# Performance work log

Hardware: AMD Instinct MI355X
Metric: run time of the kernel (lower is better)

The kernel has to match this reference:

```python
import jax, jax.numpy as jnp
import numpy as np

M = 1024      # mol_dim
H = 1024      # ffn_hidden
T = 2048      # sequence length
NS = 5        # n_solvents
DE = 64       # desc_emb_dim
NB = 3        # ffn/residual blocks
HIN = 2 * M + DE + 1  # beta head input dim


def setup_inputs() -> dict:
    key = jax.random.key(0)
    ks = jax.random.split(key, 32)
    w = lambda i, shape: (0.02 * jax.random.normal(ks[i], shape, dtype=jnp.float32))
    inp = {
        "mol_vec": jax.random.normal(ks[0], (M,), dtype=jnp.float32),
        "solvent_seq": jax.random.uniform(ks[1], (T, NS), dtype=jnp.float32),
        "desc_seq": jax.random.normal(ks[2], (T, 6), dtype=jnp.float32),
        "solvent_vecs": jax.random.normal(ks[3], (NS, M), dtype=jnp.float32),
        "boundary_mask": jnp.zeros((T,), dtype=bool),
        # SolventProjection: Linear(5*M -> M) + 3 residual FFN blocks
        "sp_proj_w": w(4, (NS * M, M)), "sp_proj_b": jnp.zeros((M,), jnp.float32),
        "sp_fc1_w": w(5, (NB, M, M)), "sp_fc1_b": jnp.zeros((NB, M), jnp.float32),
        "sp_fc2_w": w(6, (NB, M, M)), "sp_fc2_b": jnp.zeros((NB, M), jnp.float32),
        "sp_ln_g": jnp.ones((NB, M), jnp.float32), "sp_ln_b": jnp.zeros((NB, M), jnp.float32),
        # desc_proj: Linear(6 -> 64)
        "desc_w": w(7, (6, DE)), "desc_b": jnp.zeros((DE,), jnp.float32),
        "bh_proj_w": w(8, (HIN, H)), "bh_proj_b": jnp.zeros((H,), jnp.float32),
        "bh_fc1_w": w(9, (NB, H, H)), "bh_fc1_b": jnp.zeros((NB, H), jnp.float32),
        "bh_fc2_w": w(10, (NB, H, H)), "bh_fc2_b": jnp.zeros((NB, H), jnp.float32),
        "bh_ln_g": jnp.ones((NB, H), jnp.float32), "bh_ln_b": jnp.zeros((NB, H), jnp.float32),
        "mu_w": w(11, (H,)), "mu_b": jnp.zeros((1,), jnp.float32),
        "phi_w": w(12, (H,)), "phi_b": jnp.zeros((1,), jnp.float32),
    }
    return inp


def _gelu(x):
    return jax.nn.gelu(x, approximate=False)  # torch nn.GELU default (erf)


def _ln(x, g, b, eps=1e-5):
    m = jnp.mean(x, axis=-1, keepdims=True)
    v = jnp.mean((x - m) ** 2, axis=-1, keepdims=True)
    return g * (x - m) * jax.lax.rsqrt(v + eps) + b


def _res_blocks(x, w1, b1, w2, b2, g, b):
    # stack of ResidualFFNBlock (dropout=0 / eval mode)
    for i in range(w1.shape[0]):
        x = _ln(_gelu(x @ w1[i] + b1[i]) @ w2[i] + b2[i] + x, g[i], b[i])
    return x


def reference(mol_vec, solvent_seq, desc_seq, solvent_vecs, boundary_mask,
              sp_proj_w, sp_proj_b, sp_fc1_w, sp_fc1_b, sp_fc2_w, sp_fc2_b, sp_ln_g, sp_ln_b,
              desc_w, desc_b,
              bh_proj_w, bh_proj_b, bh_fc1_w, bh_fc1_b, bh_fc2_w, bh_fc2_b, bh_ln_g, bh_ln_b,
              mu_w, mu_b, phi_w, phi_b):
    def step(prev_rf, xs):
        ratios, desc, is_b = xs  # [5], [6], scalar bool
        # SolventProjection: scale each solvent vec by its ratio, concat, project
        sv = (solvent_vecs * ratios[:, None]).reshape(-1)         # [5*M]
        sp = _gelu(sv @ sp_proj_w + sp_proj_b)                     # [M]
        sp = _res_blocks(sp, sp_fc1_w, sp_fc1_b, sp_fc2_w, sp_fc2_b, sp_ln_g, sp_ln_b)
        demb = _gelu(desc @ desc_w + desc_b)                       # [DE]
        x = jnp.concatenate([mol_vec, sp, demb, prev_rf[None]])   # [HIN]
        z = _gelu(x @ bh_proj_w + bh_proj_b)                       # [H]
        z = _res_blocks(z, bh_fc1_w, bh_fc1_b, bh_fc2_w, bh_fc2_b, bh_ln_g, bh_ln_b)
        mu = jax.nn.sigmoid(jnp.dot(z, mu_w) + mu_b[0])
        phi = jax.nn.softplus(jnp.dot(z, phi_w) + phi_b[0]) + 2.0
        # monotonic update: restart at system boundaries or before first prediction
        rf = jnp.where(is_b | (prev_rf < 0), mu, prev_rf + mu * (1.0 - prev_rf))
        return jax.lax.stop_gradient(rf), (rf, mu, phi)  # prev_rf is detached in torch

    prev0 = jnp.float32(-1.0)
    _, (rfs, mus, phis) = jax.lax.scan(step, prev0, (solvent_seq, desc_seq, boundary_mask))
    return jnp.stack([rfs, mus, phis])  # [3, T]
```

## Files before the change

### kernel.cpp

```cpp
#include <hip/hip_runtime.h>
#include <math.h>

#define MDIM 1024
#define TSEQ 2048
#define NSOL 5
#define DED  64
#define NBLK 3
#define KITER 2
#define XLDB 1088
#define NRED 14336
#define RST  64

typedef __bf16 bf16x8 __attribute__((ext_vector_type(8)));
typedef __bf16 bf16x4 __attribute__((ext_vector_type(4)));
typedef float  f32x4  __attribute__((ext_vector_type(4)));

#define GLDS16(gptr, lptr) __builtin_amdgcn_global_load_lds( \
    (const __attribute__((address_space(1))) unsigned int*)(const void*)(gptr), \
    (__attribute__((address_space(3))) unsigned int*)(void*)(lptr), 16, 0, 0)

__device__ __forceinline__ float gelu_f(float x){
  return 0.5f * x * (1.0f + erff(x * 0.70710678118654752440f));
}
__device__ __forceinline__ float sigmoid_f(float x){ return 1.0f/(1.0f+expf(-x)); }
__device__ __forceinline__ float softplus_f(float x){ return fmaxf(x,0.0f) + log1pf(expf(-fabsf(x))); }

__global__ __launch_bounds__(256) void k_cvtT13(const float* __restrict__ s0,
    const float* __restrict__ s1, const float* __restrict__ s2, const float* __restrict__ s3,
    const float* __restrict__ s4, __bf16* __restrict__ dst, __bf16* __restrict__ WpT,
    const float* __restrict__ spg, const float* __restrict__ bhg){
  __shared__ float t[32][33];
  const size_t MM = (size_t)MDIM*MDIM;
  int z = blockIdx.z;
  int tx = threadIdx.x & 31, ty = threadIdx.x >> 5;
  if (z < 12){
    if (blockIdx.y >= 32) return;
    const float* s = (z<3)? s0 + (size_t)z*MM : (z<6)? s1 + (size_t)(z-3)*MM :
                     (z<9)? s2 + (size_t)(z-6)*MM : s3 + (size_t)(z-9)*MM;
    const float* gf = (z==1)? spg : (z==2)? spg+MDIM : (z==7)? bhg : (z==8)? bhg+MDIM : nullptr;
    __bf16* d = dst + (size_t)z*MM;
    int k0 = blockIdx.y*32, n0 = blockIdx.x*32;
    #pragma unroll
    for (int r=0;r<32;r+=8){
      float val = s[(size_t)(k0+ty+r)*MDIM + n0+tx];
      if (gf) val *= gf[k0+ty+r];
      t[ty+r][tx] = val;
    }
    __syncthreads();
    #pragma unroll
    for (int r=0;r<32;r+=8) d[(size_t)(n0+ty+r)*MDIM + k0+tx] = (__bf16)t[tx][ty+r];
  } else {
    int k0 = blockIdx.y*32, n0 = blockIdx.x*32;
    #pragma unroll
    for (int r=0;r<32;r+=8) t[ty+r][tx] = s4[(size_t)(k0+ty+r)*MDIM + n0+tx];
    __syncthreads();
    #pragma unroll
    for (int r=0;r<32;r+=8) WpT[(size_t)(n0+ty+r)*XLDB + k0+tx] = (__bf16)t[tx][ty+r];
  }
}

__global__ __launch_bounds__(256) void k_pm(const float* __restrict__ sv,
    const float* __restrict__ spW, const float* __restrict__ mol,
    const float* __restrict__ bhw, float* __restrict__ PART,
    const float* __restrict__ spfc1w, const float* __restrict__ bhfc1w,
    const float* __restrict__ splg, const float* __restrict__ splb,
    const float* __restrict__ bhlg, const float* __restrict__ bhlb){
  const size_t MM = (size_t)MDIM*MDIM;
  int s = blockIdx.y;
  int j = blockIdx.x*256 + threadIdx.x;
  int z = blockIdx.z, k0 = z*64;
  if (s < NSOL){
    const float* w = spW + (size_t)s*MM + (size_t)k0*MDIM + j;
    const float* v = sv + s*MDIM + k0;
    float acc = 0.f;
    for (int k=0;k<64;k++) acc = fmaf(v[k], w[(size_t)k*MDIM], acc);
    PART[(size_t)z*NRED + s*MDIM + j] = acc;
  } else if (s == NSOL){
    const float* w = bhw + (size_t)k0*MDIM + j;
    float acc = 0.f;
    for (int k=0;k<64;k++) acc = fmaf(mol[k0+k], w[(size_t)k*MDIM], acc);
    PART[(size_t)z*NRED + 5120 + j] = acc;
  } else {
    int m = s - 6;
    const float* W = (m<2)? spfc1w + (size_t)(m+1)*MM : bhfc1w + (size_t)(m-1)*MM;
    const float* g = (m<2)? splg + m*MDIM : bhlg + (m-2)*MDIM;
    const float* b = (m<2)? splb + m*MDIM : bhlb + (m-2)*MDIM;
    float aS=0.f, aB=0.f;
    for (int k=0;k<64;k++){
      float w = W[(size_t)(k0+k)*MDIM + j];
      aS = fmaf(g[k0+k], w, aS);
      aB = fmaf(b[k0+k], w, aB);
    }
    PART[(size_t)z*NRED + 6144 + m*2048 + j] = aS;
    PART[(size_t)z*NRED + 6144 + m*2048 + 1024 + j] = aB;
  }
}

__global__ __launch_bounds__(256) void k_red(const float* __restrict__ PART,
    const float* __restrict__ bhb, float* __restrict__ P, float* __restrict__ mp,
    float* __restrict__ prevg, int* __restrict__ dlist, int* __restrict__ dcnt,
    const float* __restrict__ spfc1b, const float* __restrict__ bhfc1b,
    float* __restrict__ S1buf, float* __restrict__ biasF){
  int i = blockIdx.x*256 + threadIdx.x;
  if (i < TSEQ){ prevg[i] = (i==0)? -1.0f : 1.0f; dlist[i] = i; }
  if (i == 0) *dcnt = TSEQ;
  float a = 0.f;
  #pragma unroll
  for (int z=0;z<16;z++) a += PART[(size_t)z*NRED + i];
  if (i < 5120) P[i] = a;
  else if (i < 6144) mp[i-5120] = a + bhb[i-5120];
  else {
    int off = i - 6144, m = off>>11, r = off&2047;
    if (r < 1024) S1buf[(m<<10)+r] = a;
    else {
      const float* b1 = ((m<2)? spfc1b : bhfc1b) + (((m&1)+1)<<10);
      biasF[(m<<10)+(r-1024)] = a + b1[r-1024];
    }
  }
}

__global__ __launch_bounds__(256) void k_sp0d(const float* __restrict__ ratios,
    const float* __restrict__ P, const float* __restrict__ bias,
    const float* __restrict__ desc, const float* __restrict__ dw,
    const float* __restrict__ db, __bf16* __restrict__ Xb){
  int t = blockIdx.y;
  if (blockIdx.x < 4){
    int j = blockIdx.x*256 + threadIdx.x;
    const float* r = ratios + t*NSOL;
    float acc = bias[j];
    #pragma unroll
    for (int s=0;s<NSOL;s++) acc = fmaf(r[s], P[s*MDIM+j], acc);
    Xb[(size_t)t*XLDB + j] = (__bf16)gelu_f(acc);
  } else if (threadIdx.x < DED){
    int e = threadIdx.x;
    const float* d = desc + t*6;
    float acc = db[e];
    #pragma unroll
    for (int c=0;c<6;c++) acc = fmaf(d[c], dw[c*DED+e], acc);
    Xb[(size_t)t*XLDB + MDIM + e] = (__bf16)gelu_f(acc);
  }
}

template<int BK, bool GELU, bool RES, bool RESLN, bool OUTF, bool OUTB, bool Z0, bool LNFOLD, bool STATS>
__global__ __launch_bounds__(512) void k_mfma_gemm(
    const __bf16* __restrict__ A, int lda, int K,
    const __bf16* __restrict__ Bt,
    const float* __restrict__ bias,
    const __bf16* __restrict__ R, int ldr,
    float* __restrict__ Cf, int ldcf,
    __bf16* __restrict__ Cb, int ldcb,
    const float* __restrict__ wlast, const float* __restrict__ prevg,
    __bf16* __restrict__ Z0b,
    const float* __restrict__ pSin, const float* __restrict__ pQin,
    float* __restrict__ pSout, float* __restrict__ pQout,
    const float* __restrict__ S1, const float* __restrict__ biasF,
    const float* __restrict__ lng, const float* __restrict__ lnb)
{
  constexpr int CPR = BK/8;
  constexpr int AG  = BK/32;
  constexpr int BG  = (BK>=64)? BK/64 : 1;
  constexpr int KS  = BK/32;
  constexpr int VPS = AG + BG;
  __shared__ __attribute__((aligned(16))) __bf16 As[3][128*BK];
  __shared__ __attribute__((aligned(16))) __bf16 Bs[3][64*BK];
  __shared__ float srowS[128], srowQ[128];
  __shared__ float sr2S[2][128], sr2Q[2][128];
  int tid = threadIdx.x;
  int wave = tid>>6, lane = tid&63;
  int nlin = blockIdx.y*16 + blockIdx.x;
  int kq = nlin>>3;
  int by = 2*(nlin&7) + (kq>>4), bx = kq&15;
  int row0 = by*128, col0 = bx*64;
  int wr = (wave>>1)*32, wc = (wave&1)*32;
  int lr = lane&15;
  f32x4 acc[2][2] = {};
  int NT = K / BK;

  auto stage = [&](int b, int k0){
    #pragma unroll
    for (int p=0;p<AG;p++){
      int q = wave*(AG*64) + p*64 + lane;
      int r = q/CPR, c = q%CPR, cl = c^(r&7);
      GLDS16(A + (size_t)(row0+r)*lda + k0 + cl*8, &As[b][(wave*(AG*64)+p*64)*8]);
    }
    #pragma unroll
    for (int p=0;p<BG;p++){
      int q = wave*(BG*64) + p*64 + lane;
      int r = q/CPR, c = q%CPR, cl = c^(r&7);
      GLDS16(Bt + (size_t)(col0+r)*K + k0 + cl*8, &Bs[b][(wave*(BG*64)+p*64)*8]);
    }
  };

  stage(0, 0);
  if (NT > 1) stage(1, BK);
  if (LNFOLD || RESLN){
    if (tid < 128){
      float a=0.f, b2=0.f;
      #pragma unroll
      for (int x2=0;x2<16;x2++){
        a  += pSin[x2*2048 + row0 + tid];
        b2 += pQin[x2*2048 + row0 + tid];
      }
      srowS[tid]=a; srowQ[tid]=b2;
    }
    __syncthreads();
  }
  for (int t=0; t<NT; t++){
    if (t+1 < NT) asm volatile("s_waitcnt vmcnt(%0)" :: "i"(VPS) : "memory");
    else          asm volatile("s_waitcnt vmcnt(0)" ::: "memory");
    __builtin_amdgcn_s_barrier();
    asm volatile("" ::: "memory");
    if (t+2 < NT) stage((t+2)%3, (t+2)*BK);
    int b = t%3;
    #pragma unroll
    for (int ks=0;ks<KS;ks++){
      int c = ks*4 + (lane>>4);
      bf16x8 af[2], bg[2];
      #pragma unroll
      for (int m=0;m<2;m++){
        int rowA = wr + m*16 + lr;
        af[m] = *(const bf16x8*)&As[b][rowA*BK + ((c ^ (rowA&7))<<3)];
      }
      #pragma unroll
      for (int n=0;n<2;n++){
        int rowB = wc + n*16 + lr;
        bg[n] = *(const bf16x8*)&Bs[b][rowB*BK + ((c ^ (rowB&7))<<3)];
      }
      #pragma unroll
      for (int m=0;m<2;m++)
        #pragma unroll
        for (int n=0;n<2;n++)
          acc[m][n] = __builtin_amdgcn_mfma_f32_16x16x32_bf16(af[m], bg[n], acc[m][n], 0,0,0);
    }
  }
  int rq = (lane>>4)*4;
  float sst[2][4], ssq[2][4];
  if (STATS){
    #pragma unroll
    for (int m=0;m<2;m++)
      #pragma unroll
      for (int q=0;q<4;q++){ sst[m][q]=0.f; ssq[m][q]=0.f; }
  }
  #pragma unroll
  for (int m=0;m<2;m++){
    #pragma unroll
    for (int n=0;n<2;n++){
      int cc = col0 + wc + n*16 + lr;
      float bv  = LNFOLD ? 0.f : bias[cc];
      float s1v = LNFOLD ? S1[cc] : 0.f;
      float bfv = LNFOLD ? biasF[cc] : 0.f;
      float gcc = RESLN ? lng[cc] : 0.f;
      float bcc = RESLN ? lnb[cc] : 0.f;
      #pragma unroll
      for (int q=0;q<4;q++){
        int r = row0 + wr + m*16 + rq + q;
        int rl = r - row0;
        float v = acc[m][n][q];
        if (LNFOLD){
          float s = srowS[rl], q2 = srowQ[rl];
          float mean = s*(1.0f/MDIM);
          float var  = q2*(1.0f/MDIM) - mean*mean;
          float rs   = rsqrtf(var + 1e-5f);
          v = rs*v - rs*mean*s1v + bfv;
          v = gelu_f(v);
        } else {
          v += bv;
          if (RES) v += (float)R[(size_t)r*ldr + cc];
          if (RESLN){
            float s = srowS[rl], q2 = srowQ[rl];
            float mean = s*(1.0f/MDIM);
            float var  = q2*(1.0f/MDIM) - mean*mean;
            float rs   = rsqrtf(var + 1e-5f);
            v += gcc*((float)R[(size_t)r*ldr + cc] - mean)*rs + bcc;
          }
          if (GELU) v = gelu_f(v);
        }
        if (STATS){ sst[m][q] += v; ssq[m][q] += v*v; }
        if (OUTF) Cf[(size_t)r*ldcf + cc] = v;
        if (OUTB) Cb[(size_t)r*ldcb + cc] = (__bf16)v;
        if (Z0)   Z0b[(size_t)r*MDIM + cc] = (__bf16)gelu_f(v + prevg[r]*wlast[cc]);
      }
    }
  }
  if (STATS){
    #pragma unroll
    for (int off=1; off<16; off<<=1){
      #pragma unroll
      for (int m=0;m<2;m++)
        #pragma unroll
        for (int q=0;q<4;q++){
          sst[m][q] += __shfl_xor(sst[m][q], off);
          ssq[m][q] += __shfl_xor(ssq[m][q], off);
        }
    }
    if ((lane&15)==0){
      #pragma unroll
      for (int m=0;m<2;m++)
        #pragma unroll
        for (int q=0;q<4;q++){
          int rl = wr + m*16 + rq + q;
          sr2S[wave&1][rl] = sst[m][q];
          sr2Q[wave&1][rl] = ssq[m][q];
        }
    }
    __syncthreads();
    if (tid < 128){
      pSout[bx*2048 + row0 + tid] = sr2S[0][tid] + sr2S[1][tid];
      pQout[bx*2048 + row0 + tid] = sr2Q[0][tid] + sr2Q[1][tid];
    }
  }
}

template<bool MUPHI>
__global__ __launch_bounds__(256) void k_ln(const float* __restrict__ Y, int ldy,
    __bf16* __restrict__ Xb, int ldxb,
    const float* __restrict__ g, const float* __restrict__ b,
    const float* __restrict__ muw, const float* __restrict__ mub,
    const float* __restrict__ phiw, const float* __restrict__ phib,
    float* __restrict__ muA, float* __restrict__ phiA)
{
  int t = blockIdx.x;
  __shared__ float red[16];
  int tid = threadIdx.x;
  f32x4 y = *(const f32x4*)&Y[(size_t)t*ldy + tid*4];
  float s  = y[0]+y[1]+y[2]+y[3];
  float s2 = y[0]*y[0]+y[1]*y[1]+y[2]*y[2]+y[3]*y[3];
  for (int o=32;o>0;o>>=1){ s += __shfl_down(s,o); s2 += __shfl_down(s2,o); }
  int wid = tid>>6, lane = tid&63;
  if (lane==0){ red[wid]=s; red[wid+8]=s2; }
  __syncthreads();
  if (tid==0){
    float a=0.f,c=0.f;
    for (int w=0;w<4;w++){ a+=red[w]; c+=red[w+8]; }
    red[0]=a; red[8]=c;
  }
  __syncthreads();
  float mean = red[0]*(1.0f/MDIM);
  float var  = red[8]*(1.0f/MDIM) - mean*mean;
  float rs = rsqrtf(var + 1e-5f);
  f32x4 gv = *(const f32x4*)&g[tid*4];
  f32x4 bb = *(const f32x4*)&b[tid*4];
  f32x4 v; bf16x4 vb;
  #pragma unroll
  for (int i=0;i<4;i++){ v[i] = gv[i]*(y[i]-mean)*rs + bb[i]; vb[i] = (__bf16)v[i]; }
  *(bf16x4*)&Xb[(size_t)t*ldxb + tid*4] = vb;
  if (MUPHI){
    f32x4 mw = *(const f32x4*)&muw[tid*4];
    f32x4 pw = *(const f32x4*)&phiw[tid*4];
    float sm=0.f, sp=0.f;
    #pragma unroll
    for (int i=0;i<4;i++){ sm = fmaf(v[i], mw[i], sm); sp = fmaf(v[i], pw[i], sp); }
    for (int o=32;o>0;o>>=1){ sm+=__shfl_down(sm,o); sp+=__shfl_down(sp,o); }
    __syncthreads();
    if (lane==0){ red[wid]=sm; red[wid+8]=sp; }
    __syncthreads();
    if (tid==0){
      float a=0.f,c=0.f;
      for (int w=0;w<4;w++){ a+=red[w]; c+=red[w+8]; }
      muA[t]  = sigmoid_f(a + mub[0]);
      phiA[t] = softplus_f(c + phib[0]) + 2.0f;
    }
  }
}


__global__ __launch_bounds__(64) void k_fc1z_dirty(
    const float* __restrict__ ZP, const float* __restrict__ wlast,
    const float* __restrict__ prevg,
    const __bf16* __restrict__ Wt, const float* __restrict__ bias,
    const int* __restrict__ dlist, const int* __restrict__ dcnt,
    __bf16* __restrict__ Zb, __bf16* __restrict__ Ob)
{
  __shared__ __bf16 zl[MDIM];
  int nd = *dcnt;
  int jb = blockIdx.x;
  int j = jb*64 + threadIdx.x;
  for (int rs = blockIdx.y; rs < nd; rs += RST){
    int t = dlist[rs];
    float prev = prevg[t];
    #pragma unroll
    for (int q=0;q<16;q++){
      int k = threadIdx.x + 64*q;
      __bf16 v = (__bf16)gelu_f(ZP[(size_t)t*MDIM + k] + prev*wlast[k]);
      zl[k] = v;
      if (jb==0) Zb[(size_t)t*MDIM + k] = v;
    }
    __syncthreads();
    const __bf16* w = Wt + (size_t)j*MDIM;
    float acc = 0.f;
    for (int k=0;k<MDIM;k+=8){
      bf16x8 wv = *(const bf16x8*)&w[k];
      bf16x8 iv = *(const bf16x8*)&zl[k];
      #pragma unroll
// ... 81 lines not shown
    const float* __restrict__ phiw, const float* __restrict__ phib,
    float* __restrict__ muA, float* __restrict__ phiA)
{
  int nd = *dcnt;
  for (int rs = blockIdx.x; rs < nd; rs += RST){
    int t = dlist[rs];
    float y[16]; float s=0.f, s2=0.f;
    #pragma unroll
    for (int q=0;q<16;q++){
      y[q] = Y[(size_t)t*MDIM + threadIdx.x + 64*q];
      s += y[q]; s2 += y[q]*y[q];
    }
    for (int o=32;o>0;o>>=1){ s += __shfl_down(s,o); s2 += __shfl_down(s2,o); }
    float tot  = __shfl(s, 0);
    float tot2 = __shfl(s2, 0);
    float mean = tot*(1.0f/MDIM);
    float var  = tot2*(1.0f/MDIM) - mean*mean;
    float rs2 = rsqrtf(var + 1e-5f);
    float sm=0.f, sp=0.f;
    #pragma unroll
    for (int q=0;q<16;q++){
      int k = threadIdx.x + 64*q;
      float v = g[k]*(y[q]-mean)*rs2 + b[k];
      sm = fmaf(v, muw[k], sm); sp = fmaf(v, phiw[k], sp);
    }
    for (int o=32;o>0;o>>=1){ sm+=__shfl_down(sm,o); sp+=__shfl_down(sp,o); }
    if (threadIdx.x==0){
      muA[t]  = sigmoid_f(sm + mub[0]);
      phiA[t] = softplus_f(sp + phib[0]) + 2.0f;
    }
  }
}

__global__ __launch_bounds__(1024) void k_scan(
    const float* __restrict__ muA, const float* __restrict__ phiA,
    const unsigned char* __restrict__ bmask,
    float* __restrict__ prevg, int* __restrict__ dlist, int* __restrict__ dcnt,
    float* __restrict__ out)
{
  if (*dcnt == 0) return;
  __shared__ float aggP[16];
  __shared__ unsigned aggF[16];
  __shared__ float wprP[16];
  __shared__ unsigned wprF[16];
  __shared__ int cnt;
  int tid = threadIdx.x;
  int wid = tid>>6, lane = tid&63;
  if (tid==0) cnt = 0;
  int i0 = wid*128 + lane*2;
  float mu0 = muA[i0], mu1 = muA[i0+1];
  float p0 = 1.0f - mu0, p1 = 1.0f - mu1;
  unsigned f0 = (i0==0) || (bmask[i0] != 0);
  unsigned f1 = (bmask[i0+1] != 0);
  float    sp_ = f1 ? p1 : p0*p1;
  unsigned sf_ = f0|f1;
  #pragma unroll
  for (int off=1; off<64; off<<=1){
    float    op = __shfl_up(sp_, off);
    unsigned of = __shfl_up(sf_, off);
    if (lane >= off && !sf_){ sp_ = op*sp_; sf_ = of; }
  }
  if (lane==63){ aggP[wid]=sp_; aggF[wid]=sf_; }
  __syncthreads();
  if (wid==0 && lane<16){
    float ap = aggP[lane]; unsigned af = aggF[lane];
    #pragma unroll
    for (int off=1; off<16; off<<=1){
      float    op = __shfl_up(ap, off);
      unsigned of = __shfl_up(af, off);
      if (lane >= off && !af){ ap = op*ap; af = of; }
    }
    wprP[lane]=ap; wprF[lane]=af;
  }
  __syncthreads();
  float    wpP = (wid==0)? 1.0f : wprP[wid-1];
  float    lpP = __shfl_up(sp_, 1);
  unsigned lpF = __shfl_up(sf_, 1);
  float exP;
  if (lane==0){ exP = wpP; }
  else        { exP = lpF ? lpP : wpP*lpP; }
  float i0P = f0 ? p0 : exP*p0;
  float i1P = f1 ? p1 : i0P*p1;
  float prev0 = (i0==0)? -1.0f : (1.0f - exP);
  float prev1 = 1.0f - i0P;
  float rf0 = 1.0f - i0P, rf1 = 1.0f - i1P;
  out[i0]   = rf0;  out[i0+1]   = rf1;
  out[TSEQ+i0] = mu0; out[TSEQ+i0+1] = mu1;
  out[2*TSEQ+i0] = phiA[i0]; out[2*TSEQ+i0+1] = phiA[i0+1];
  float old0 = prevg[i0], old1 = prevg[i0+1];
  prevg[i0] = prev0; prevg[i0+1] = prev1;
  if (fabsf(prev0 - old0) > 1e-3f){ int pos = atomicAdd(&cnt,1); dlist[pos] = i0; }
  if (fabsf(prev1 - old1) > 1e-3f){ int pos = atomicAdd(&cnt,1); dlist[pos] = i0+1; }
  __syncthreads();
  if (tid==0) *dcnt = cnt;
}

extern "C" void kernel_launch(void* const* d_in, const int* in_sizes, int n_in,
                              void* d_out, int out_size, void* d_ws, size_t ws_size,
                              hipStream_t stream) {
  const float* mol       = (const float*)d_in[0];
  const float* ratios    = (const float*)d_in[1];
  const float* desc      = (const float*)d_in[2];
  const float* svvec     = (const float*)d_in[3];
  const unsigned char* bmask = (const unsigned char*)d_in[4];
  const float* sp_proj_w = (const float*)d_in[5];
  const float* sp_proj_b = (const float*)d_in[6];
  const float* sp_fc1_w  = (const float*)d_in[7];
  const float* sp_fc1_b  = (const float*)d_in[8];
  const float* sp_fc2_w  = (const float*)d_in[9];
  const float* sp_fc2_b  = (const float*)d_in[10];
  const float* sp_ln_g   = (const float*)d_in[11];
  const float* sp_ln_b   = (const float*)d_in[12];
  const float* desc_w    = (const float*)d_in[13];
  const float* desc_b    = (const float*)d_in[14];
  const float* bh_proj_w = (const float*)d_in[15];
  const float* bh_proj_b = (const float*)d_in[16];
  const float* bh_fc1_w  = (const float*)d_in[17];
  const float* bh_fc1_b  = (const float*)d_in[18];
  const float* bh_fc2_w  = (const float*)d_in[19];
  const float* bh_fc2_b  = (const float*)d_in[20];
  const float* bh_ln_g   = (const float*)d_in[21];
  const float* bh_ln_b   = (const float*)d_in[22];
  const float* mu_w      = (const float*)d_in[23];
  const float* mu_b      = (const float*)d_in[24];
  const float* phi_w     = (const float*)d_in[25];
  const float* phi_b     = (const float*)d_in[26];
  float* out = (float*)d_out;

  char* p = (char*)d_ws;
  auto alloc = [&](size_t bytes)->char*{ char* r = p; p += (bytes + 255) & ~(size_t)255; return r; };
  const size_t MM = (size_t)MDIM*MDIM;
  __bf16* Xb   = (__bf16*)alloc((size_t)TSEQ*XLDB*2);
  __bf16* Zb   = (__bf16*)alloc((size_t)TSEQ*MDIM*2);
  __bf16* Yb0  = (__bf16*)alloc((size_t)TSEQ*MDIM*2);
  __bf16* Yb1  = (__bf16*)alloc((size_t)TSEQ*MDIM*2);
  float*  Y    = (float*)alloc((size_t)TSEQ*MDIM*4);
  float*  ZP   = (float*)alloc((size_t)TSEQ*MDIM*4);
  __bf16* Hb16 = (__bf16*)alloc((size_t)TSEQ*MDIM*2);
  __bf16* WALL = (__bf16*)alloc(12*MM*2);
  __bf16* WpT  = (__bf16*)alloc((size_t)MDIM*XLDB*2);
  float*  PART = (float*)alloc((size_t)16*NRED*4);
  float*  P    = (float*)alloc((size_t)NSOL*MDIM*4);
  float*  mp   = (float*)alloc(MDIM*4);
  float*  prevg= (float*)alloc(TSEQ*4);
  float*  muA  = (float*)alloc(TSEQ*4);
  float*  phiA = (float*)alloc(TSEQ*4);
  int*    dlist= (int*)alloc(TSEQ*4);
  int*    dcnt = (int*)alloc(256);
  float*  pAS  = (float*)alloc((size_t)16*2048*4);
  float*  pAQ  = (float*)alloc((size_t)16*2048*4);
  float*  pBS  = (float*)alloc((size_t)16*2048*4);
  float*  pBQ  = (float*)alloc((size_t)16*2048*4);
  float*  S1buf= (float*)alloc(4*MDIM*4);
  float*  biasF= (float*)alloc(4*MDIM*4);
  __bf16* W1T = WALL, *W2T = WALL + 3*MM, *U1T = WALL + 6*MM, *U2T = WALL + 9*MM;

  k_cvtT13<<<dim3(32,34,13),256,0,stream>>>(sp_fc1_w, sp_fc2_w, bh_fc1_w, bh_fc2_w,
      bh_proj_w + MM, WALL, WpT, sp_ln_g, bh_ln_g);
  k_pm<<<dim3(4,10,16),256,0,stream>>>(svvec, sp_proj_w, mol, bh_proj_w, PART,
      sp_fc1_w, bh_fc1_w, sp_ln_g, sp_ln_b, bh_ln_g, bh_ln_b);
  k_red<<<dim3(NRED/256),256,0,stream>>>(PART, bh_proj_b, P, mp, prevg, dlist, dcnt,
      sp_fc1_b, bh_fc1_b, S1buf, biasF);
  k_sp0d<<<dim3(5,TSEQ),256,0,stream>>>(ratios, P, sp_proj_b, desc, desc_w, desc_b, Xb);

  const float* wlast = bh_proj_w + (size_t)2112*MDIM;
  dim3 gg(16,16);
  k_mfma_gemm<128,true,false,false,false,true,false,false,false><<<gg,512,0,stream>>>(
      Xb, XLDB, 1024, W1T, sp_fc1_b, nullptr, 0, nullptr, 0, Hb16, MDIM,
      nullptr, nullptr, nullptr, nullptr, nullptr, nullptr, nullptr, nullptr, nullptr, nullptr, nullptr);
  k_mfma_gemm<128,false,true,false,false,true,false,false,true><<<gg,512,0,stream>>>(
      Hb16, MDIM, 1024, W2T, sp_fc2_b, Xb, XLDB, nullptr, 0, Yb0, MDIM,
      nullptr, nullptr, nullptr, nullptr, nullptr, pAS, pAQ, nullptr, nullptr, nullptr, nullptr);
  k_mfma_gemm<128,false,false,false,false,true,false,true,false><<<gg,512,0,stream>>>(
      Yb0, MDIM, 1024, W1T + 1*MM, nullptr, nullptr, 0, nullptr, 0, Hb16, MDIM,
      nullptr, nullptr, nullptr, pAS, pAQ, nullptr, nullptr, S1buf, biasF, nullptr, nullptr);
  k_mfma_gemm<128,false,false,true,false,true,false,false,true><<<gg,512,0,stream>>>(
      Hb16, MDIM, 1024, W2T + 1*MM, sp_fc2_b + 1024, Yb0, MDIM, nullptr, 0, Yb1, MDIM,
      nullptr, nullptr, nullptr, pAS, pAQ, pBS, pBQ, nullptr, nullptr, sp_ln_g, sp_ln_b);
  k_mfma_gemm<128,false,false,false,false,true,false,true,false><<<gg,512,0,stream>>>(
      Yb1, MDIM, 1024, W1T + 2*MM, nullptr, nullptr, 0, nullptr, 0, Hb16, MDIM,
      nullptr, nullptr, nullptr, pBS, pBQ, nullptr, nullptr, S1buf + 1024, biasF + 1024, nullptr, nullptr);
  k_mfma_gemm<128,false,false,true,true,false,false,false,false><<<gg,512,0,stream>>>(
      Hb16, MDIM, 1024, W2T + 2*MM, sp_fc2_b + 2048, Yb1, MDIM, Y, MDIM, nullptr, 0,
      nullptr, nullptr, nullptr, pBS, pBQ, nullptr, nullptr, nullptr, nullptr, sp_ln_g + 1024, sp_ln_b + 1024);
  k_ln<false><<<dim3(TSEQ),256,0,stream>>>(Y, MDIM, Xb, XLDB,
      sp_ln_g + 2048, sp_ln_b + 2048, nullptr, nullptr, nullptr, nullptr, nullptr, nullptr);
  k_mfma_gemm<64,false,false,false,true,false,true,false,false><<<gg,512,0,stream>>>(
      Xb, XLDB, XLDB, WpT, mp, nullptr, 0, ZP, MDIM, nullptr, 0,
      wlast, prevg, Zb, nullptr, nullptr, nullptr, nullptr, nullptr, nullptr, nullptr, nullptr);
  k_mfma_gemm<128,true,false,false,false,true,false,false,false><<<gg,512,0,stream>>>(
      Zb, MDIM, 1024, U1T, bh_fc1_b, nullptr, 0, nullptr, 0, Hb16, MDIM,
      nullptr, nullptr, nullptr, nullptr, nullptr, nullptr, nullptr, nullptr, nullptr, nullptr, nullptr);
  k_mfma_gemm<128,false,true,false,false,true,false,false,true><<<gg,512,0,stream>>>(
      Hb16, MDIM, 1024, U2T, bh_fc2_b, Zb, MDIM, nullptr, 0, Yb0, MDIM,
      nullptr, nullptr, nullptr, nullptr, nullptr, pAS, pAQ, nullptr, nullptr, nullptr, nullptr);
  k_mfma_gemm<128,false,false,false,false,true,false,true,false><<<gg,512,0,stream>>>(
      Yb0, MDIM, 1024, U1T + 1*MM, nullptr, nullptr, 0, nullptr, 0, Hb16, MDIM,
      nullptr, nullptr, nullptr, pAS, pAQ, nullptr, nullptr, S1buf + 2048, biasF + 2048, nullptr, nullptr);
  k_mfma_gemm<128,false,false,true,false,true,false,false,true><<<gg,512,0,stream>>>(
      Hb16, MDIM, 1024, U2T + 1*MM, bh_fc2_b + 1024, Yb0, MDIM, nullptr, 0, Yb1, MDIM,
      nullptr, nullptr, nullptr, pAS, pAQ, pBS, pBQ, nullptr, nullptr, bh_ln_g, bh_ln_b);
  k_mfma_gemm<128,false,false,false,false,true,false,true,false><<<gg,512,0,stream>>>(
      Yb1, MDIM, 1024, U1T + 2*MM, nullptr, nullptr, 0, nullptr, 0, Hb16, MDIM,
      nullptr, nullptr, nullptr, pBS, pBQ, nullptr, nullptr, S1buf + 3072, biasF + 3072, nullptr, nullptr);
  k_mfma_gemm<128,false,false,true,true,false,false,false,false><<<gg,512,0,stream>>>(
      Hb16, MDIM, 1024, U2T + 2*MM, bh_fc2_b + 2048, Yb1, MDIM, Y, MDIM, nullptr, 0,
      nullptr, nullptr, nullptr, pBS, pBQ, nullptr, nullptr, nullptr, nullptr, bh_ln_g + 1024, bh_ln_b + 1024);
  k_ln<true><<<dim3(TSEQ),256,0,stream>>>(Y, MDIM, Zb, MDIM,
      bh_ln_g + 2048, bh_ln_b + 2048, mu_w, mu_b, phi_w, phi_b, muA, phiA);
  k_scan<<<dim3(1),1024,0,stream>>>(muA, phiA, bmask, prevg, dlist, dcnt, out);

  for (int it=1; it<KITER; it++){
    k_fc1z_dirty<<<dim3(16,RST),64,0,stream>>>(ZP, wlast, prevg,
        U1T, bh_fc1_b, dlist, dcnt, Zb, Hb16);
    k_fc2_dirty<<<dim3(16,RST),64,0,stream>>>(
        Hb16, U2T, bh_fc2_b, Zb, dlist, dcnt, Y);
    for (int i=1;i<NBLK;i++){
      k_lnfc1_dirty<<<dim3(16,RST),64,0,stream>>>(Y,
          bh_ln_g + (i-1)*MDIM, bh_ln_b + (i-1)*MDIM,
          U1T + (size_t)i*MM, biasF + (i+1)*MDIM, dlist, dcnt, Zb, Hb16);
      k_fc2_dirty<<<dim3(16,RST),64,0,stream>>>(
          Hb16, U2T + (size_t)i*MM, bh_fc2_b + i*MDIM, Zb, dlist, dcnt, Y);
    }
    k_lnmp_dirty<<<dim3(RST),64,0,stream>>>(Y,
        bh_ln_g + (NBLK-1)*MDIM, bh_ln_b + (NBLK-1)*MDIM,
        dlist, dcnt, mu_w, mu_b, phi_w, phi_b, muA, phiA);
    k_scan<<<dim3(1),1024,0,stream>>>(muA, phiA, bmask, prevg, dlist, dcnt, out);
  }
  (void)in_sizes; (void)n_in; (void)out_size; (void)ws_size;
}
```

Baseline: 355.3 us.

## Fold final LayerNorms into GEMM epilogues and scan, removing standalone LN kernels

Removes the two standalone LayerNorm passes. The solvent branch's last LN is folded into the beta-head projection GEMM: the LN gamma is pre-multiplied into the projection weights, and row mean/variance come from the fc2 epilogue statistics. The mol/desc/prev part of that GEMM goes into a separate accumulator so the LN correction only applies to the folded part. The head's last LN and the mu/phi dot products are folded into the last fc2 epilogue (per-row dot partials with gamma-scaled head weights) and finished in the first scan. This avoids writing and rereading the full fp32 activation matrix twice, at the cost of extra registers, epilogue work and more complex numerics.

```diff
diff --git a/kernel.cpp b/kernel.cpp
--- a/kernel.cpp
+++ b/kernel.cpp
@@ -8,7 +8,7 @@
 #define NBLK 3
 #define KITER 2
 #define XLDB 1088
-#define NRED 14336
+#define NRED 16384
 #define RST  64
 
 typedef __bf16 bf16x8 __attribute__((ext_vector_type(8)));
@@ -28,7 +28,8 @@
 __global__ __launch_bounds__(256) void k_cvtT13(const float* __restrict__ s0,
     const float* __restrict__ s1, const float* __restrict__ s2, const float* __restrict__ s3,
     const float* __restrict__ s4, __bf16* __restrict__ dst, __bf16* __restrict__ WpT,
-    const float* __restrict__ spg, const float* __restrict__ bhg){
+    const float* __restrict__ spg, const float* __restrict__ bhg,
+    const float* __restrict__ spg3){
   __shared__ float t[32][33];
   const size_t MM = (size_t)MDIM*MDIM;
   int z = blockIdx.z;
@@ -52,7 +53,12 @@
   } else {
     int k0 = blockIdx.y*32, n0 = blockIdx.x*32;
     #pragma unroll
-    for (int r=0;r<32;r+=8) t[ty+r][tx] = s4[(size_t)(k0+ty+r)*MDIM + n0+tx];
+    for (int r=0;r<32;r+=8){
+      int kk = k0+ty+r;
+      float val = s4[(size_t)kk*MDIM + n0+tx];
+      if (kk < 1024) val *= spg3[kk];
+      t[ty+r][tx] = val;
+    }
     __syncthreads();
     #pragma unroll
     for (int r=0;r<32;r+=8) WpT[(size_t)(n0+ty+r)*XLDB + k0+tx] = (__bf16)t[tx][ty+r];
@@ -82,9 +88,10 @@
     PART[(size_t)z*NRED + 5120 + j] = acc;
   } else {
     int m = s - 6;
-    const float* W = (m<2)? spfc1w + (size_t)(m+1)*MM : bhfc1w + (size_t)(m-1)*MM;
-    const float* g = (m<2)? splg + m*MDIM : bhlg + (m-2)*MDIM;
-    const float* b = (m<2)? splb + m*MDIM : bhlb + (m-2)*MDIM;
+    const float* W = (m<2)? spfc1w + (size_t)(m+1)*MM :
+                     (m<4)? bhfc1w + (size_t)(m-1)*MM : bhw + MM;
+    const float* g = (m<2)? splg + m*MDIM : (m<4)? bhlg + (m-2)*MDIM : splg + 2*MDIM;
+    const float* b = (m<2)? splb + m*MDIM : (m<4)? bhlb + (m-2)*MDIM : splb + 2*MDIM;
     float aS=0.f, aB=0.f;
     for (int k=0;k<64;k++){
       float w = W[(size_t)(k0+k)*MDIM + j];
@@ -100,21 +107,50 @@
     const float* __restrict__ bhb, float* __restrict__ P, float* __restrict__ mp,
     float* __restrict__ prevg, int* __restrict__ dlist, int* __restrict__ dcnt,
     const float* __restrict__ spfc1b, const float* __restrict__ bhfc1b,
-    float* __restrict__ S1buf, float* __restrict__ biasF){
-  int i = blockIdx.x*256 + threadIdx.x;
-  if (i < TSEQ){ prevg[i] = (i==0)? -1.0f : 1.0f; dlist[i] = i; }
-  if (i == 0) *dcnt = TSEQ;
-  float a = 0.f;
-  #pragma unroll
-  for (int z=0;z<16;z++) a += PART[(size_t)z*NRED + i];
-  if (i < 5120) P[i] = a;
-  else if (i < 6144) mp[i-5120] = a + bhb[i-5120];
-  else {
-    int off = i - 6144, m = off>>11, r = off&2047;
-    if (r < 1024) S1buf[(m<<10)+r] = a;
+    float* __restrict__ S1buf, float* __restrict__ biasF,
+    const float* __restrict__ lng3, const float* __restrict__ lnb3,
+    const float* __restrict__ muw, const float* __restrict__ mub,
+    const float* __restrict__ phiw, const float* __restrict__ phib,
+    float* __restrict__ gmuwF, float* __restrict__ gphiwF, float* __restrict__ scal){
+  if (blockIdx.x < 64){
+    int i = blockIdx.x*256 + threadIdx.x;
+    if (i < TSEQ){ prevg[i] = (i==0)? -1.0f : 1.0f; dlist[i] = i; }
+    if (i == 0) *dcnt = TSEQ;
+    float a = 0.f;
+    #pragma unroll
+    for (int z=0;z<16;z++) a += PART[(size_t)z*NRED + i];
+    if (i < 5120) P[i] = a;
+    else if (i < 6144) mp[i-5120] = a + bhb[i-5120];
     else {
-      const float* b1 = ((m<2)? spfc1b : bhfc1b) + (((m&1)+1)<<10);
-      biasF[(m<<10)+(r-1024)] = a + b1[r-1024];
+      int off = i - 6144, m = off>>11, r = off&2047;
+      if (r < 1024) S1buf[(m<<10)+r] = a;
+      else if (m < 4){
+        const float* b1 = ((m<2)? spfc1b : bhfc1b) + (((m&1)+1)<<10);
+        biasF[(m<<10)+(r-1024)] = a + b1[r-1024];
+      } else biasF[(m<<10)+(r-1024)] = a;
+    }
+  } else {
+    __shared__ float red[16];
+    int wid = threadIdx.x>>6, lane = threadIdx.x&63;
+    float lS1=0.f,lS2=0.f,lC1=0.f,lC2=0.f;
+    #pragma unroll
+    for (int u=0;u<4;u++){
+      int j = threadIdx.x*4+u;
+      float g = lng3[j], b = lnb3[j], mw = muw[j], pw = phiw[j];
+      float gm = g*mw, gp = g*pw;
+      gmuwF[j]=gm; gphiwF[j]=gp;
+      lS1+=gm; lS2+=gp; lC1+=b*mw; lC2+=b*pw;
+    }
+    for (int o=32;o>0;o>>=1){
+      lS1+=__shfl_down(lS1,o); lS2+=__shfl_down(lS2,o);
+      lC1+=__shfl_down(lC1,o); lC2+=__shfl_down(lC2,o);
+    }
+    if (lane==0){ red[wid]=lS1; red[wid+4]=lS2; red[wid+8]=lC1; red[wid+12]=lC2; }
+    __syncthreads();
+    if (threadIdx.x==0){
+      float a=0.f,b2=0.f,c=0.f,d=0.f;
+      for (int w=0;w<4;w++){ a+=red[w]; b2+=red[4+w]; c+=red[8+w]; d+=red[12+w]; }
+      scal[0]=a; scal[1]=b2; scal[2]=c+mub[0]; scal[3]=d+phib[0];
     }
   }
 }
@@ -154,7 +190,9 @@
     const float* __restrict__ pSin, const float* __restrict__ pQin,
     float* __restrict__ pSout, float* __restrict__ pQout,
     const float* __restrict__ S1, const float* __restrict__ biasF,
-    const float* __restrict__ lng, const float* __restrict__ lnb)
+    const float* __restrict__ lng, const float* __restrict__ lnb,
+    float* __restrict__ pD1out, float* __restrict__ pD2out,
+    const float* __restrict__ gmw, const float* __restrict__ gpw)
 {
   constexpr int CPR = BK/8;
   constexpr int AG  = BK/32;
@@ -165,6 +203,7 @@
   __shared__ __attribute__((aligned(16))) __bf16 Bs[3][64*BK];
   __shared__ float srowS[128], srowQ[128];
   __shared__ float sr2S[2][128], sr2Q[2][128];
+  __shared__ float sr2D1[2][128], sr2D2[2][128];
   int tid = threadIdx.x;
   int wave = tid>>6, lane = tid&63;
   int nlin = blockIdx.y*16 + blockIdx.x;
@@ -174,6 +213,7 @@
   int wr = (wave>>1)*32, wc = (wave&1)*32;
   int lr = lane&15;
   f32x4 acc[2][2] = {};
+  f32x4 accB[2][2] = {};
   int NT = K / BK;
 
   auto stage = [&](int b, int k0){
@@ -188,6 +228,28 @@
       int q = wave*(BG*64) + p*64 + lane;
       int r = q/CPR, c = q%CPR, cl = c^(r&7);
       GLDS16(Bt + (size_t)(col0+r)*K + k0 + cl*8, &Bs[b][(wave*(BG*64)+p*64)*8]);
+    }
+  };
+  auto compute = [&](f32x4 (&ac)[2][2], int b){
+    #pragma unroll
+    for (int ks=0;ks<KS;ks++){
+      int c = ks*4 + (lane>>4);
+      bf16x8 af[2], bg[2];
+      #pragma unroll
+      for (int m=0;m<2;m++){
+        int rowA = wr + m*16 + lr;
+        af[m] = *(const bf16x8*)&As[b][rowA*BK + ((c ^ (rowA&7))<<3)];
+      }
+      #pragma unroll
+      for (int n=0;n<2;n++){
+        int rowB = wc + n*16 + lr;
+        bg[n] = *(const bf16x8*)&Bs[b][rowB*BK + ((c ^ (rowB&7))<<3)];
+      }
+      #pragma unroll
+      for (int m=0;m<2;m++)
+        #pragma unroll
+        for (int n=0;n<2;n++)
+          ac[m][n] = __builtin_amdgcn_mfma_f32_16x16x32_bf16(af[m], bg[n], ac[m][n], 0,0,0);
     }
   };
 
@@ -212,34 +274,16 @@
     asm volatile("" ::: "memory");
     if (t+2 < NT) stage((t+2)%3, (t+2)*BK);
     int b = t%3;
-    #pragma unroll
-    for (int ks=0;ks<KS;ks++){
-      int c = ks*4 + (lane>>4);
-      bf16x8 af[2], bg[2];
-      #pragma unroll
-      for (int m=0;m<2;m++){
-        int rowA = wr + m*16 + lr;
-        af[m] = *(const bf16x8*)&As[b][rowA*BK + ((c ^ (rowA&7))<<3)];
-      }
-      #pragma unroll
-      for (int n=0;n<2;n++){
-        int rowB = wc + n*16 + lr;
-        bg[n] = *(const bf16x8*)&Bs[b][rowB*BK + ((c ^ (rowB&7))<<3)];
-      }
-      #pragma unroll
-      for (int m=0;m<2;m++)
-        #pragma unroll
-        for (int n=0;n<2;n++)
-          acc[m][n] = __builtin_amdgcn_mfma_f32_16x16x32_bf16(af[m], bg[n], acc[m][n], 0,0,0);
-    }
+    if (Z0 && LNFOLD && t == NT-1) compute(accB, b);
+    else                           compute(acc, b);
   }
   int rq = (lane>>4)*4;
-  float sst[2][4], ssq[2][4];
+  float sst[2][4], ssq[2][4], sd1[2][4], sd2[2][4];
   if (STATS){
     #pragma unroll
     for (int m=0;m<2;m++)
       #pragma unroll
-      for (int q=0;q<4;q++){ sst[m][q]=0.f; ssq[m][q]=0.f; }
+      for (int q=0;q<4;q++){ sst[m][q]=0.f; ssq[m][q]=0.f; sd1[m][q]=0.f; sd2[m][q]=0.f; }
   }
   #pragma unroll
   for (int m=0;m<2;m++){
@@ -251,6 +295,8 @@
       float bfv = LNFOLD ? biasF[cc] : 0.f;
       float gcc = RESLN ? lng[cc] : 0.f;
       float bcc = RESLN ? lnb[cc] : 0.f;
+      float gmv = (STATS && pD1out) ? gmw[cc] : 0.f;
+      float gpv = (STATS && pD1out) ? gpw[cc] : 0.f;
       #pragma unroll
       for (int q=0;q<4;q++){
         int r = row0 + wr + m*16 + rq + q;
@@ -262,7 +308,8 @@
           float var  = q2*(1.0f/MDIM) - mean*mean;
           float rs   = rsqrtf(var + 1e-5f);
           v = rs*v - rs*mean*s1v + bfv;
-          v = gelu_f(v);
+          if (Z0) v += bias[cc] + accB[m][n][q];
+          if (GELU) v = gelu_f(v);
         } else {
           v += bv;
           if (RES) v += (float)R[(size_t)r*ldr + cc];
@@ -275,7 +322,10 @@
           }
           if (GELU) v = gelu_f(v);
         }
-        if (STATS){ sst[m][q] += v; ssq[m][q] += v*v; }
+        if (STATS){
+          sst[m][q] += v; ssq[m][q] += v*v;
+          if (pD1out){ sd1[m][q] += v*gmv; sd2[m][q] += v*gpv; }
+        }
         if (OUTF) Cf[(size_t)r*ldcf + cc] = v;
         if (OUTB) Cb[(size_t)r*ldcb + cc] = (__bf16)v;
         if (Z0)   Z0b[(size_t)r*MDIM + cc] = (__bf16)gelu_f(v + prevg[r]*wlast[cc]);
@@ -291,6 +341,8 @@
         for (int q=0;q<4;q++){
           sst[m][q] += __shfl_xor(sst[m][q], off);
           ssq[m][q] += __shfl_xor(ssq[m][q], off);
+          sd1[m][q] += __shfl_xor(sd1[m][q], off);
+          sd2[m][q] += __shfl_xor(sd2[m][q], off);
         }
     }
     if ((lane&15)==0){
@@ -301,64 +353,18 @@
           int rl = wr + m*16 + rq + q;
           sr2S[wave&1][rl] = sst[m][q];
           sr2Q[wave&1][rl] = ssq[m][q];
+          sr2D1[wave&1][rl] = sd1[m][q];
+          sr2D2[wave&1][rl] = sd2[m][q];
         }
     }
     __syncthreads();
     if (tid < 128){
       pSout[bx*2048 + row0 + tid] = sr2S[0][tid] + sr2S[1][tid];
       pQout[bx*2048 + row0 + tid] = sr2Q[0][tid] + sr2Q[1][tid];
-    }
-  }
-}
-
-template<bool MUPHI>
-__global__ __launch_bounds__(256) void k_ln(const float* __restrict__ Y, int ldy,
-    __bf16* __restrict__ Xb, int ldxb,
-    const float* __restrict__ g, const float* __restrict__ b,
-    const float* __restrict__ muw, const float* __restrict__ mub,
-    const float* __restrict__ phiw, const float* __restrict__ phib,
-    float* __restrict__ muA, float* __restrict__ phiA)
-{
-  int t = blockIdx.x;
-  __shared__ float red[16];
-  int tid = threadIdx.x;
-  f32x4 y = *(const f32x4*)&Y[(size_t)t*ldy + tid*4];
-  float s  = y[0]+y[1]+y[2]+y[3];
-  float s2 = y[0]*y[0]+y[1]*y[1]+y[2]*y[2]+y[3]*y[3];
-  for (int o=32;o>0;o>>=1){ s += __shfl_down(s,o); s2 += __shfl_down(s2,o); }
-  int wid = tid>>6, lane = tid&63;
-  if (lane==0){ red[wid]=s; red[wid+8]=s2; }
-  __syncthreads();
-  if (tid==0){
-    float a=0.f,c=0.f;
-    for (int w=0;w<4;w++){ a+=red[w]; c+=red[w+8]; }
-    red[0]=a; red[8]=c;
-  }
-  __syncthreads();
-  float mean = red[0]*(1.0f/MDIM);
-  float var  = red[8]*(1.0f/MDIM) - mean*mean;
-  float rs = rsqrtf(var + 1e-5f);
-  f32x4 gv = *(const f32x4*)&g[tid*4];
-  f32x4 bb = *(const f32x4*)&b[tid*4];
-  f32x4 v; bf16x4 vb;
-  #pragma unroll
-  for (int i=0;i<4;i++){ v[i] = gv[i]*(y[i]-mean)*rs + bb[i]; vb[i] = (__bf16)v[i]; }
-  *(bf16x4*)&Xb[(size_t)t*ldxb + tid*4] = vb;
-  if (MUPHI){
-    f32x4 mw = *(const f32x4*)&muw[tid*4];
-    f32x4 pw = *(const f32x4*)&phiw[tid*4];
-    float sm=0.f, sp=0.f;
-    #pragma unroll
-    for (int i=0;i<4;i++){ sm = fmaf(v[i], mw[i], sm); sp = fmaf(v[i], pw[i], sp); }
-    for (int o=32;o>0;o>>=1){ sm+=__shfl_down(sm,o); sp+=__shfl_down(sp,o); }
-    __syncthreads();
-    if (lane==0){ red[wid]=sm; red[wid+8]=sp; }
-    __syncthreads();
-    if (tid==0){
-      float a=0.f,c=0.f;
-      for (int w=0;w<4;w++){ a+=red[w]; c+=red[w+8]; }
-      muA[t]  = sigmoid_f(a + mub[0]);
-      phiA[t] = softplus_f(c + phib[0]) + 2.0f;
+      if (pD1out){
+        pD1out[bx*2048 + row0 + tid] = sr2D1[0][tid] + sr2D1[1][tid];
+        pD2out[bx*2048 + row0 + tid] = sr2D2[0][tid] + sr2D2[1][tid];
+      }
     }
   }
 }
@@ -506,13 +512,17 @@
   }
 }
 
+template<bool FIRST>
 __global__ __launch_bounds__(1024) void k_scan(
-    const float* __restrict__ muA, const float* __restrict__ phiA,
+    const float* __restrict__ muA_in, float* __restrict__ muA, float* __restrict__ phiA,
     const unsigned char* __restrict__ bmask,
     float* __restrict__ prevg, int* __restrict__ dlist, int* __restrict__ dcnt,
-    float* __restrict__ out)
+    float* __restrict__ out,
+    const float* __restrict__ pS, const float* __restrict__ pQ,
+    const float* __restrict__ pD1, const float* __restrict__ pD2,
+    const float* __restrict__ scal)
 {
-  if (*dcnt == 0) return;
+  if (!FIRST && *dcnt == 0) return;
   __shared__ float aggP[16];
   __shared__ unsigned aggF[16];
   __shared__ float wprP[16];
@@ -522,7 +532,25 @@
   int wid = tid>>6, lane = tid&63;
   if (tid==0) cnt = 0;
   int i0 = wid*128 + lane*2;
-  float mu0 = muA[i0], mu1 = muA[i0+1];
+  float mu0, mu1, ph0, ph1;
+  if (FIRST){
+    float S1m = scal[0], S2m = scal[1], C1 = scal[2], C2 = scal[3];
+    float s0=0.f,q0=0.f,d10=0.f,d20=0.f, s1=0.f,q1=0.f,d11=0.f,d21=0.f;
+    for (int x=0;x<16;x++){
+      s0+=pS[x*2048+i0];  q0+=pQ[x*2048+i0];  d10+=pD1[x*2048+i0];  d20+=pD2[x*2048+i0];
+      s1+=pS[x*2048+i0+1];q1+=pQ[x*2048+i0+1];d11+=pD1[x*2048+i0+1];d21+=pD2[x*2048+i0+1];
+    }
+    float m0 = s0*(1.0f/MDIM), v0 = q0*(1.0f/MDIM)-m0*m0, r0 = rsqrtf(v0+1e-5f);
+    float m1 = s1*(1.0f/MDIM), v1 = q1*(1.0f/MDIM)-m1*m1, r1 = rsqrtf(v1+1e-5f);
+    mu0 = sigmoid_f(r0*(d10 - m0*S1m) + C1);
+    ph0 = softplus_f(r0*(d20 - m0*S2m) + C2) + 2.0f;
+    mu1 = sigmoid_f(r1*(d11 - m1*S1m) + C1);
+    ph1 = softplus_f(r1*(d21 - m1*S2m) + C2) + 2.0f;
+    muA[i0]=mu0; muA[i0+1]=mu1; phiA[i0]=ph0; phiA[i0+1]=ph1;
+  } else {
+    mu0 = muA_in[i0]; mu1 = muA_in[i0+1];
+    ph0 = phiA[i0];   ph1 = phiA[i0+1];
+  }
   float p0 = 1.0f - mu0, p1 = 1.0f - mu1;
   unsigned f0 = (i0==0) || (bmask[i0] != 0);
   unsigned f1 = (bmask[i0+1] != 0);
@@ -560,7 +588,7 @@
   float rf0 = 1.0f - i0P, rf1 = 1.0f - i1P;
   out[i0]   = rf0;  out[i0+1]   = rf1;
   out[TSEQ+i0] = mu0; out[TSEQ+i0+1] = mu1;
-  out[2*TSEQ+i0] = phiA[i0]; out[2*TSEQ+i0+1] = phiA[i0+1];
+  out[2*TSEQ+i0] = ph0; out[2*TSEQ+i0+1] = ph1;
   float old0 = prevg[i0], old1 = prevg[i0+1];
   prevg[i0] = prev0; prevg[i0+1] = prev1;
   if (fabsf(prev0 - old0) > 1e-3f){ int pos = atomicAdd(&cnt,1); dlist[pos] = i0; }
@@ -625,64 +653,80 @@
   float*  pAQ  = (float*)alloc((size_t)16*2048*4);
   float*  pBS  = (float*)alloc((size_t)16*2048*4);
   float*  pBQ  = (float*)alloc((size_t)16*2048*4);
-  float*  S1buf= (float*)alloc(4*MDIM*4);
-  float*  biasF= (float*)alloc(4*MDIM*4);
+  float*  pD1  = (float*)alloc((size_t)16*2048*4);
+  float*  pD2  = (float*)alloc((size_t)16*2048*4);
+  float*  S1buf= (float*)alloc(5*MDIM*4);
+  float*  biasF= (float*)alloc(5*MDIM*4);
+  float*  gmuwF= (float*)alloc(MDIM*4);
+  float*  gphiwF=(float*)alloc(MDIM*4);
+  float*  scal = (float*)alloc(256);
   __bf16* W1T = WALL, *W2T = WALL + 3*MM, *U1T = WALL + 6*MM, *U2T = WALL + 9*MM;
 
   k_cvtT13<<<dim3(32,34,13),256,0,stream>>>(sp_fc1_w, sp_fc2_w, bh_fc1_w, bh_fc2_w,
-      bh_proj_w + MM, WALL, WpT, sp_ln_g, bh_ln_g);
-  k_pm<<<dim3(4,10,16),256,0,stream>>>(svvec, sp_proj_w, mol, bh_proj_w, PART,
+      bh_proj_w + MM, WALL, WpT, sp_ln_g, bh_ln_g, sp_ln_g + 2048);
+  k_pm<<<dim3(4,11,16),256,0,stream>>>(svvec, sp_proj_w, mol, bh_proj_w, PART,
       sp_fc1_w, bh_fc1_w, sp_ln_g, sp_ln_b, bh_ln_g, bh_ln_b);
-  k_red<<<dim3(NRED/256),256,0,stream>>>(PART, bh_proj_b, P, mp, prevg, dlist, dcnt,
-      sp_fc1_b, bh_fc1_b, S1buf, biasF);
+  k_red<<<dim3(65),256,0,stream>>>(PART, bh_proj_b, P, mp, prevg, dlist, dcnt,
+      sp_fc1_b, bh_fc1_b, S1buf, biasF,
+      bh_ln_g + 2048, bh_ln_b + 2048, mu_w, mu_b, phi_w, phi_b, gmuwF, gphiwF, scal);
   k_sp0d<<<dim3(5,TSEQ),256,0,stream>>>(ratios, P, sp_proj_b, desc, desc_w, desc_b, Xb);
 
   const float* wlast = bh_proj_w + (size_t)2112*MDIM;
   dim3 gg(16,16);
   k_mfma_gemm<128,true,false,false,false,true,false,false,false><<<gg,512,0,stream>>>(
       Xb, XLDB, 1024, W1T, sp_fc1_b, nullptr, 0, nullptr, 0, Hb16, MDIM,
-      nullptr, nullptr, nullptr, nullptr, nullptr, nullptr, nullptr, nullptr, nullptr, nullptr, nullptr);
+      nullptr, nullptr, nullptr, nullptr, nullptr, nullptr, nullptr, nullptr, nullptr, nullptr, nullptr,
+      nullptr, nullptr, nullptr, nullptr);
   k_mfma_gemm<128,false,true,false,false,true,false,false,true><<<gg,512,0,stream>>>(
       Hb16, MDIM, 1024, W2T, sp_fc2_b, Xb, XLDB, nullptr, 0, Yb0, MDIM,
-      nullptr, nullptr, nullptr, nullptr, nullptr, pAS, pAQ, nullptr, nullptr, nullptr, nullptr);
-  k_mfma_gemm<128,false,false,false,false,true,false,true,false><<<gg,512,0,stream>>>(
+      nullptr, nullptr, nullptr, nullptr, nullptr, pAS, pAQ, nullptr, nullptr, nullptr, nullptr,
+      nullptr, nullptr, nullptr, nullptr);
+  k_mfma_gemm<128,true,false,false,false,true,false,true,false><<<gg,512,0,stream>>>(
       Yb0, MDIM, 1024, W1T + 1*MM, nullptr, nullptr, 0, nullptr, 0, Hb16, MDIM,
-      nullptr, nullptr, nullptr, pAS, pAQ, nullptr, nullptr, S1buf, biasF, nullptr, nullptr);
+      nullptr, nullptr, nullptr, pAS, pAQ, nullptr, nullptr, S1buf, biasF, nullptr, nullptr,
+      nullptr, nullptr, nullptr, nullptr);
   k_mfma_gemm<128,false,false,true,false,true,false,false,true><<<gg,512,0,stream>>>(
       Hb16, MDIM, 1024, W2T + 1*MM, sp_fc2_b + 1024, Yb0, MDIM, nullptr, 0, Yb1, MDIM,
-      nullptr, nullptr, nullptr, pAS, pAQ, pBS, pBQ, nullptr, nullptr, sp_ln_g, sp_ln_b);
-  k_mfma_gemm<128,false,false,false,false,true,false,true,false><<<gg,512,0,stream>>>(
+      nullptr, nullptr, nullptr, pAS, pAQ, pBS, pBQ, nullptr, nullptr, sp_ln_g, sp_ln_b,
+      nullptr, nullptr, nullptr, nullptr);
+  k_mfma_gemm<128,true,false,false,false,true,false,true,false><<<gg,512,0,stream>>>(
       Yb1, MDIM, 1024, W1T + 2*MM, nullptr, nullptr, 0, nullptr, 0, Hb16, MDIM,
-      nullptr, nullptr, nullptr, pBS, pBQ, nullptr, nullptr, S1buf + 1024, biasF + 1024, nullptr, nullptr);
-  k_mfma_gemm<128,false,false,true,true,false,false,false,false><<<gg,512,0,stream>>>(
-      Hb16, MDIM, 1024, W2T + 2*MM, sp_fc2_b + 2048, Yb1, MDIM, Y, MDIM, nullptr, 0,
-      nullptr, nullptr, nullptr, pBS, pBQ, nullptr, nullptr, nullptr, nullptr, sp_ln_g + 1024, sp_ln_b + 1024);
-  k_ln<false><<<dim3(TSEQ),256,0,stream>>>(Y, MDIM, Xb, XLDB,
-      sp_ln_g + 2048, sp_ln_b + 2048, nullptr, nullptr, nullptr, nullptr, nullptr, nullptr);
-  k_mfma_gemm<64,false,false,false,true,false,true,false,false><<<gg,512,0,stream>>>(
+      nullptr, nullptr, nullptr, pBS, pBQ, nullptr, nullptr, S1buf + 1024, biasF + 1024, nullptr, nullptr,
+      nullptr, nullptr, nullptr, nullptr);
+  k_mfma_gemm<128,false,false,true,false,true,false,false,true><<<gg,512,0,stream>>>(
+      Hb16, MDIM, 1024, W2T + 2*MM, sp_fc2_b + 2048, Yb1, MDIM, nullptr, 0, Xb, XLDB,
+      nullptr, nullptr, nullptr, pBS, pBQ, pAS, pAQ, nullptr, nullptr, sp_ln_g + 1024, sp_ln_b + 1024,
+      nullptr, nullptr, nullptr, nullptr);
+  k_mfma_gemm<64,false,false,false,true,false,true,true,false><<<gg,512,0,stream>>>(
       Xb, XLDB, XLDB, WpT, mp, nullptr, 0, ZP, MDIM, nullptr, 0,
-      wlast, prevg, Zb, nullptr, nullptr, nullptr, nullptr, nullptr, nullptr, nullptr, nullptr);
+      wlast, prevg, Zb, pAS, pAQ, nullptr, nullptr, S1buf + 4096, biasF + 4096, nullptr, nullptr,
+      nullptr, nullptr, nullptr, nullptr);
   k_mfma_gemm<128,true,false,false,false,true,false,false,false><<<gg,512,0,stream>>>(
       Zb, MDIM, 1024, U1T, bh_fc1_b, nullptr, 0, nullptr, 0, Hb16, MDIM,
-      nullptr, nullptr, nullptr, nullptr, nullptr, nullptr, nullptr, nullptr, nullptr, nullptr, nullptr);
+      nullptr, nullptr, nullptr, nullptr, nullptr, nullptr, nullptr, nullptr, nullptr, nullptr, nullptr,
+      nullptr, nullptr, nullptr, nullptr);
   k_mfma_gemm<128,false,true,false,false,true,false,false,true><<<gg,512,0,stream>>>(
       Hb16, MDIM, 1024, U2T, bh_fc2_b, Zb, MDIM, nullptr, 0, Yb0, MDIM,
-      nullptr, nullptr, nullptr, nullptr, nullptr, pAS, pAQ, nullptr, nullptr, nullptr, nullptr);
-  k_mfma_gemm<128,false,false,false,false,true,false,true,false><<<gg,512,0,stream>>>(
+      nullptr, nullptr, nullptr, nullptr, nullptr, pBS, pBQ, nullptr, nullptr, nullptr, nullptr,
+      nullptr, nullptr, nullptr, nullptr);
+  k_mfma_gemm<128,true,false,false,false,true,false,true,false><<<gg,512,0,stream>>>(
       Yb0, MDIM, 1024, U1T + 1*MM, nullptr, nullptr, 0, nullptr, 0, Hb16, MDIM,
-      nullptr, nullptr, nullptr, pAS, pAQ, nullptr, nullptr, S1buf + 2048, biasF + 2048, nullptr, nullptr);
+      nullptr, nullptr, nullptr, pBS, pBQ, nullptr, nullptr, S1buf + 2048, biasF + 2048, nullptr, nullptr,
+      nullptr, nullptr, nullptr, nullptr);
   k_mfma_gemm<128,false,false,true,false,true,false,false,true><<<gg,512,0,stream>>>(
       Hb16, MDIM, 1024, U2T + 1*MM, bh_fc2_b + 1024, Yb0, MDIM, nullptr, 0, Yb1, MDIM,
-      nullptr, nullptr, nullptr, pAS, pAQ, pBS, pBQ, nullptr, nullptr, bh_ln_g, bh_ln_b);
-  k_mfma_gemm<128,false,false,false,false,true,false,true,false><<<gg,512,0,stream>>>(
+      nullptr, nullptr, nullptr, pBS, pBQ, pAS, pAQ, nullptr, nullptr, bh_ln_g, bh_ln_b,
+      nullptr, nullptr, nullptr, nullptr);
+  k_mfma_gemm<128,true,false,false,false,true,false,true,false><<<gg,512,0,stream>>>(
       Yb1, MDIM, 1024, U1T + 2*MM, nullptr, nullptr, 0, nullptr, 0, Hb16, MDIM,
-      nullptr, nullptr, nullptr, pBS, pBQ, nullptr, nullptr, S1buf + 3072, biasF + 3072, nullptr, nullptr);
-  k_mfma_gemm<128,false,false,true,true,false,false,false,false><<<gg,512,0,stream>>>(
-      Hb16, MDIM, 1024, U2T + 2*MM, bh_fc2_b + 2048, Yb1, MDIM, Y, MDIM, nullptr, 0,
-      nullptr, nullptr, nullptr, pBS, pBQ, nullptr, nullptr, nullptr, nullptr, bh_ln_g + 1024, bh_ln_b + 1024);
-  k_ln<true><<<dim3(TSEQ),256,0,stream>>>(Y, MDIM, Zb, MDIM,
-      bh_ln_g + 2048, bh_ln_b + 2048, mu_w, mu_b, phi_w, phi_b, muA, phiA);
-  k_scan<<<dim3(1),1024,0,stream>>>(muA, phiA, bmask, prevg, dlist, dcnt, out);
+      nullptr, nullptr, nullptr, pAS, pAQ, nullptr, nullptr, S1buf + 3072, biasF + 3072, nullptr, nullptr,
+      nullptr, nullptr, nullptr, nullptr);
+  k_mfma_gemm<128,false,false,true,false,false,false,false,true><<<gg,512,0,stream>>>(
+      Hb16, MDIM, 1024, U2T + 2*MM, bh_fc2_b + 2048, Yb1, MDIM, nullptr, 0, nullptr, 0,
+      nullptr, nullptr, nullptr, pAS, pAQ, pBS, pBQ, nullptr, nullptr, bh_ln_g + 1024, bh_ln_b + 1024,
+      pD1, pD2, gmuwF, gphiwF);
+  k_scan<true><<<dim3(1),1024,0,stream>>>(muA, muA, phiA, bmask, prevg, dlist, dcnt, out,
+      pBS, pBQ, pD1, pD2, scal);
 
   for (int it=1; it<KITER; it++){
     k_fc1z_dirty<<<dim3(16,RST),64,0,stream>>>(ZP, wlast, prevg,
@@ -699,7 +743,8 @@
     k_lnmp_dirty<<<dim3(RST),64,0,stream>>>(Y,
         bh_ln_g + (NBLK-1)*MDIM, bh_ln_b + (NBLK-1)*MDIM,
         dlist, dcnt, mu_w, mu_b, phi_w, phi_b, muA, phiA);
-    k_scan<<<dim3(1),1024,0,stream>>>(muA, phiA, bmask, prevg, dlist, dcnt, out);
+    k_scan<false><<<dim3(1),1024,0,stream>>>(muA, muA, phiA, bmask, prevg, dlist, dcnt, out,
+        nullptr, nullptr, nullptr, nullptr, nullptr);
   }
   (void)in_sizes; (void)n_in; (void)out_size; (void)ws_size;
 }
```

Result: slower. 364.7 us (+2.6%).
